# Optimization experiments

Measured on AMD Instinct MI355X. Metric: run time of the kernel, lower is better.

The kernel has to match this reference:

```python
import jax, jax.numpy as jnp
import numpy as np

THRESHOLD = 0.05
TOP_N = 300
NMS_THR = 0.6
POST_TOP_N = 100
MIN_SIZE = 0
N_CLASS = 81
C = N_CLASS - 1
STRIDES = (8, 16, 32, 64, 128)
IMG_H, IMG_W = 800, 1024
B = 16


def _level_hw(s):
    return (-(-IMG_H // s), -(-IMG_W // s))


def setup_inputs() -> dict:
    key = jax.random.key(0)
    inp = {}
    for li, s in enumerate(STRIDES):
        H, W = _level_hw(s)
        key, k1, k2, k3 = jax.random.split(key, 4)
        xs = (jnp.arange(W, dtype=jnp.float32) + 0.5) * s
        ys = (jnp.arange(H, dtype=jnp.float32) + 0.5) * s
        gx, gy = jnp.meshgrid(xs, ys)  # [H, W], row-major h*W+w flatten order
        inp[f"location{li}"] = jnp.stack([gx.reshape(-1), gy.reshape(-1)], -1)
        inp[f"cls{li}"] = jax.random.normal(k1, (B, C, H, W), jnp.float32)
        inp[f"box{li}"] = jax.random.uniform(k2, (B, 4, H, W), jnp.float32) * (4.0 * s)
        inp[f"ctr{li}"] = jax.random.normal(k3, (B, 1, H, W), jnp.float32)
    inp["img_h"] = IMG_H
    inp["img_w"] = IMG_W
    return inp


def _process_level(loc, cls, box, ctr, img_h, img_w):
    b, c, h, w = cls.shape
    cls = jax.nn.sigmoid(cls.transpose(0, 2, 3, 1).reshape(b, h * w, c))
    box = box.transpose(0, 2, 3, 1).reshape(b, h * w, 4)
    ctr = jax.nn.sigmoid(ctr.reshape(b, h * w))
    score = cls * ctr[:, :, None]                 # [B, HW, C]
    masked = jnp.where(cls > THRESHOLD, score, -1.0).reshape(b, -1)
    k = min(TOP_N, masked.shape[1])
    vals, idx = jax.lax.top_k(masked, k)
    if k < TOP_N:
        vals = jnp.pad(vals, ((0, 0), (0, TOP_N - k)), constant_values=-1.0)
        idx = jnp.pad(idx, ((0, 0), (0, TOP_N - k)))
    valid = vals > 0.0                            # candidates only; pads invalid
    pos = idx // c
    label = idx % c + 1
    ssel = jnp.take_along_axis(score.reshape(b, -1), idx, axis=1)  # differentiable gather
    bsel = jnp.take_along_axis(box, pos[..., None], axis=1)        # [B, TOP_N, 4]
    lsel = loc[pos]                                                # [B, TOP_N, 2]
    # decode + clip (BoxList.clip clamps to [0, size-1])
    x1 = jnp.clip(lsel[..., 0] - bsel[..., 0], 0.0, img_w - 1.0)
    y1 = jnp.clip(lsel[..., 1] - bsel[..., 1], 0.0, img_h - 1.0)
    x2 = jnp.clip(lsel[..., 0] + bsel[..., 2], 0.0, img_w - 1.0)
    y2 = jnp.clip(lsel[..., 1] + bsel[..., 3], 0.0, img_h - 1.0)
    det = jnp.stack([x1, y1, x2, y2], -1)
    # remove_small_box: xywh with remove=1
    valid = valid & ((x2 - x1 + 1.0) >= MIN_SIZE) & ((y2 - y1 + 1.0) >= MIN_SIZE)
    scores = jnp.sqrt(jnp.maximum(ssel, 1e-12))
    return det, scores, label, valid


def _pairwise_iou(b):
    area = (b[:, 2] - b[:, 0]) * (b[:, 3] - b[:, 1])
    lt = jnp.maximum(b[:, None, :2], b[None, :, :2])
    rb = jnp.minimum(b[:, None, 2:], b[None, :, 2:])
    wh = jnp.clip(rb - lt, 0.0)
    inter = wh[..., 0] * wh[..., 1]
    union = area[:, None] + area[None, :] - inter
    return inter / jnp.maximum(union, 1e-9)


def _nms_image(boxes, scores, labels, valid, offset):
    # per-class NMS via class-offset trick: boxes of different labels never overlap
    K = boxes.shape[0]
    s = jnp.where(valid, scores, -jnp.inf)
    order = jnp.argsort(-s)
    b = boxes[order]
    v = valid[order]
    lab = labels[order]
    so = s[order]
    iou = _pairwise_iou(b + (lab.astype(b.dtype) * offset)[:, None])
    ar = jnp.arange(K)

    def body(i, keep):
        sup = (iou[i] > NMS_THR) & keep[i] & (ar > i)
        return keep & ~sup

    keep = jax.lax.fori_loop(0, K, body, v)
    s2 = jnp.where(keep, so, -jnp.inf)
    _, idx2 = jax.lax.top_k(s2, POST_TOP_N)   # post_top_n selection
    fvalid = jnp.take(keep, idx2)
    fb = jnp.where(fvalid[:, None], b[idx2], 0.0)
    fs = jnp.where(fvalid, so[idx2], 0.0)
    fl = jnp.where(fvalid, lab[idx2], 0)
    return fb, fs, fl, fvalid


def _forward(locs, clss, boxs, ctrs, img_h, img_w):
    dets, scs, labs, vals = [], [], [], []
    for loc, cl, bx, ct in zip(locs, clss, boxs, ctrs):
        d, s, l, v = _process_level(loc, cl, bx, ct, float(img_h), float(img_w))
        dets.append(d); scs.append(s); labs.append(l); vals.append(v)
    det = jnp.concatenate(dets, 1)   # [B, 5*TOP_N, 4]
    sc = jnp.concatenate(scs, 1)
    lab = jnp.concatenate(labs, 1)
    val = jnp.concatenate(vals, 1)
    offset = float(max(img_h, img_w) + 1)
    fb, fs, fl, fv = jax.vmap(lambda b_, s_, l_, v_: _nms_image(b_, s_, l_, v_, offset))(det, sc, lab, val)
    out5 = jnp.concatenate([fb, fs[..., None]], -1)  # [B, POST_TOP_N, 5]
    return out5, fl, fv


def reference(location0, location1, location2, location3, location4,
              cls0, cls1, cls2, cls3, cls4,
              box0, box1, box2, box3, box4,
              ctr0, ctr1, ctr2, ctr3, ctr4,
              img_h, img_w):
    locs = [location0, location1, location2, location3, location4]
    clss = [cls0, cls1, cls2, cls3, cls4]
    boxs = [box0, box1, box2, box3, box4]
    ctrs = [ctr0, ctr1, ctr2, ctr3, ctr4]
    return _forward(locs, clss, boxs, ctrs, img_h, img_w)
```

## Files before the change

### kernel.cpp

```cpp
#include <hip/hip_runtime.h>
#include <math.h>

#define THREADS 256

constexpr int NLEV  = 5;
constexpr int NB    = 16;
constexpr int NC    = 80;
constexpr int TOPN  = 300;
constexpr int KC    = NLEV * TOPN;
constexpr int KROWS = 1536;
constexpr int WORDS = 24;
constexpr int NTRI  = WORDS * (WORDS + 1) / 2;
constexpr int POSTN = 100;
constexpr int CAP   = 4096;
constexpr int NBINS = 2048;
constexpr int NPAIR = NLEV * NB;

constexpr int HW0 = 12800, HW1 = 3200, HW2 = 800, HW3 = 208, HW4 = 56;
constexpr int CH0 = 63, CH1 = 16, CH2 = 4, CH3 = 2, CH4 = 1;
constexpr int CHUNKS = CH0 + CH1 + CH2 + CH3 + CH4;

constexpr int GPL0 = 4000, GPL1 = 1000, GPL2 = 250, GPL3 = 65, GPL4 = 18;
constexpr int GMXB0 = 0;
constexpr int GMXB1 = GMXB0 + NB * GPL0;
constexpr int GMXB2 = GMXB1 + NB * GPL1;
constexpr int GMXB3 = GMXB2 + NB * GPL2;
constexpr int GMXB4 = GMXB3 + NB * GPL3;
constexpr int GMXN  = GMXB4 + NB * GPL4;

constexpr int BPP = 16;

constexpr int HF_BIG = 1024, HF_SMALL = 1;

constexpr size_t align256(size_t x) { return (x + 255) & ~(size_t)255; }
constexpr size_t OFF_HIST = 0;
constexpr size_t OFF_CNT  = OFF_HIST + (size_t)NPAIR * NBINS * 4;
constexpr size_t OFF_CAND = align256(OFF_CNT + (size_t)NPAIR * 4);
constexpr size_t OFF_CBOX = align256(OFF_CAND + (size_t)NPAIR * CAP * 8);
constexpr size_t OFF_CSC  = align256(OFF_CBOX + (size_t)NB * KC * 4 * 4);
constexpr size_t OFF_CLB  = align256(OFF_CSC  + (size_t)NB * KC * 4);
constexpr size_t OFF_SSC  = align256(OFF_CLB  + (size_t)NB * KC * 4);
constexpr size_t OFF_SLB  = align256(OFF_SSC  + (size_t)NB * KC * 4);
constexpr size_t OFF_SBOX = align256(OFF_SLB  + (size_t)NB * KC * 4);
constexpr size_t OFF_OBOX = align256(OFF_SBOX + (size_t)NB * KC * 4 * 4);
constexpr size_t OFF_M    = align256(OFF_OBOX + (size_t)NB * KC * 4 * 4);
constexpr size_t OFF_GMX  = align256(OFF_M + (size_t)NB * KROWS * WORDS * 8);

struct Cand { float s; int i; };

__device__ __forceinline__ float sigm(float x) { return 1.0f / (1.0f + expf(-x)); }

__device__ __forceinline__ float sigf(float x) {
#if __has_builtin(__builtin_amdgcn_exp2f) && __has_builtin(__builtin_amdgcn_rcpf)
    float e = __builtin_amdgcn_exp2f(__fmul_rn(x, -1.44269504088896340736f));
    return __builtin_amdgcn_rcpf(__fadd_rn(1.0f, e));
#else
    return 1.0f / (1.0f + __expf(-x));
#endif
}

// ... 8 lines not shown
    unsigned hi = (unsigned)__builtin_amdgcn_readlane((int)(unsigned)(v >> 32), l);
    return ((unsigned long long)hi << 32) | lo;
}

__device__ void bitonicShared(float* ss, int* si, int N) {
    for (int k = 2; k <= N; k <<= 1) {
        for (int j = k >> 1; j > 0; j >>= 1) {
            __syncthreads();
            for (int i = threadIdx.x; i < N; i += blockDim.x) {
                int ixj = i ^ j;
                if (ixj > i) {
                    float s1 = ss[i], s2 = ss[ixj];
                    int a1 = si[i], a2 = si[ixj];
                    bool bef = (s1 > s2) || (s1 == s2 && a1 < a2);
                    bool up = ((i & k) == 0);
                    if (up ? !bef : bef) { ss[i] = s2; ss[ixj] = s1; si[i] = a2; si[ixj] = a1; }
                }
            }
        }
    }
    __syncthreads();
}

__global__ __launch_bounds__(THREADS) void k_zero(unsigned* __restrict__ zp, int zn) {
    int i = blockIdx.x * THREADS + threadIdx.x;
    if (i < zn) zp[i] = 0;
}

template<int HW, int GPL, int GMXB, int HF>
__device__ __forceinline__ void histChunkV(int chunkLocal, int b,
        const float* __restrict__ cls, const float* __restrict__ ctr,
        unsigned short* __restrict__ gmx, unsigned* __restrict__ h) {
    constexpr int NE = HW * NC;
    const float* cp = cls + (size_t)b * NE;
    const float* tb = ctr + (size_t)b * HW;
    unsigned short* gp = gmx + GMXB + (size_t)b * GPL;
    int w = threadIdx.x >> 6, lane = threadIdx.x & 63;
    int half = lane >> 5, hlane = lane & 31;
    for (int bi = w; bi < 32; bi += 4) {
        int ebase = (chunkLocal * 32 + bi) * 512;
        if (ebase >= NE) break;
        int e = ebase + lane * 8;
        int kmax = 0;
        if (e < NE) {
            int c = e / HW; int hwb = e - c * HW;
            float4 xa = *(const float4*)(cp + e);
            float4 xb = *(const float4*)(cp + e + 4);
            float4 ta = *(const float4*)(tb + hwb);
            float4 tc = *(const float4*)(tb + hwb + 4);
            float xs[8] = {xa.x, xa.y, xa.z, xa.w, xb.x, xb.y, xb.z, xb.w};
            float ts[8] = {ta.x, ta.y, ta.z, ta.w, tc.x, tc.y, tc.z, tc.w};
            #pragma unroll
            for (int q = 0; q < 8; ++q) {
                float scls = sigf(xs[q]);
                float s = __fmul_rn(scls, sigf(ts[q]));
                unsigned key = scoreKey(s);
                if (key >= (unsigned)HF) atomicAdd(&h[key], 1u);
                kmax = max(kmax, (int)key);
            }
        }
        #pragma unroll
        for (int sh = 1; sh < 32; sh <<= 1) kmax = max(kmax, __shfl_xor(kmax, sh, 64));
        int g = (ebase >> 8) + half;
        if (hlane == 0 && g * 256 < NE) gp[g] = (unsigned short)kmax;
    }
}

__global__ __launch_bounds__(THREADS) void k_hist(
        const float* c0, const float* c1, const float* c2, const float* c3, const float* c4,
        const float* t0, const float* t1, const float* t2, const float* t3, const float* t4,
        unsigned short* __restrict__ gmx, unsigned* ghist) {
    __shared__ unsigned h[NBINS];
    for (int k = threadIdx.x; k < NBINS; k += THREADS) h[k] = 0;
    __syncthreads();
    int cx = blockIdx.x, b = blockIdx.y;
    int li;
    if (cx < CH0)                 { histChunkV<HW0,GPL0,GMXB0,HF_BIG>(cx, b, c0, t0, gmx, h); li = 0; }
    else if (cx < CH0+CH1)        { histChunkV<HW1,GPL1,GMXB1,HF_BIG>(cx-CH0, b, c1, t1, gmx, h); li = 1; }
    else if (cx < CH0+CH1+CH2)    { histChunkV<HW2,GPL2,GMXB2,HF_BIG>(cx-CH0-CH1, b, c2, t2, gmx, h); li = 2; }
    else if (cx < CH0+CH1+CH2+CH3){ histChunkV<HW3,GPL3,GMXB3,HF_SMALL>(cx-CH0-CH1-CH2, b, c3, t3, gmx, h); li = 3; }
    else                          { histChunkV<HW4,GPL4,GMXB4,HF_SMALL>(cx-CH0-CH1-CH2-CH3, b, c4, t4, gmx, h); li = 4; }
    __syncthreads();
    unsigned* gp = ghist + (size_t)(li * NB + b) * NBINS;
    for (int k = threadIdx.x; k < NBINS; k += THREADS) {
        unsigned v = h[k];
        if (v) atomicAdd(&gp[k], v);
    }
}

constexpr int LBUF = 1024;
constexpr int GB = 8;

template<int HW>
__device__ __forceinline__ void procList(int b, int pid, unsigned Tv, unsigned n,
        const unsigned short* __restrict__ glist,
        const float* __restrict__ cls, const float* __restrict__ ctr,
        Cand* __restrict__ cd, unsigned* __restrict__ cnt,
        Cand* __restrict__ lbuf, unsigned* __restrict__ lcnt) {
    constexpr int NE = HW * NC;
    const float* cp = cls + (size_t)b * NE;
    const float* tb = ctr + (size_t)b * HW;
    for (unsigned base = 0; base < n; base += GB) {
        float xv[GB], rv[GB];
        int ev[GB];
        bool okv[GB];
        #pragma unroll
        for (int q = 0; q < GB; ++q) {
            unsigned gi = base + q;
            int g = glist[(gi < n) ? gi : (n - 1)];
            int e = g * 256 + (int)threadIdx.x;
            bool ok = (gi < n) && (e < NE);
            e = ok ? e : 0;
// ... 4 lines not shown
            okv[q] = ok;
        }
        __builtin_amdgcn_sched_barrier(0);
        #pragma unroll
        for (int q = 0; q < GB; ++q) {
            float scls = sigm(xv[q]);
            float s = __fmul_rn(scls, sigm(rv[q]));
            unsigned key = scoreKey(s);
            bool take = okv[q] && (Tv ? (key >= Tv) : (scls > 0.05f));
            if (take) {
                int e = ev[q];
                int c = e / HW; int hw = e - c * HW;
                unsigned slot = atomicAdd(lcnt, 1u);
                if (slot < (unsigned)LBUF) { lbuf[slot].s = s; lbuf[slot].i = hw * NC + c; }
                else {
                    unsigned gs = atomicAdd(&cnt[pid], 1u);
                    if (gs < (unsigned)CAP) { cd[gs].s = s; cd[gs].i = hw * NC + c; }
                }
            }
        }
    }
}

__global__ __launch_bounds__(THREADS) void k_collect(
        const float* c0, const float* c1, const float* c2, const float* c3, const float* c4,
        const float* t0, const float* t1, const float* t2, const float* t3, const float* t4,
        const unsigned* __restrict__ ghist, const unsigned short* __restrict__ gmx,
        Cand* cand, unsigned* cnt) {
    __shared__ unsigned sfx[THREADS];
    __shared__ int tstar;
    __shared__ unsigned shTv;
    __shared__ Cand lbuf[LBUF];
    __shared__ unsigned lcnt, gbase, gcnt;
    __shared__ unsigned short glist[THREADS];
    int tid = (int)threadIdx.x;
    int pid = blockIdx.y;
    int li = pid >> 4, b = pid & 15;
    if (tid == 0) { lcnt = 0; gcnt = 0; tstar = -1; }

    const unsigned* h = ghist + (size_t)pid * NBINS;
    unsigned s = 0;
    #pragma unroll
    for (int k = 0; k < 8; ++k) s += h[tid * 8 + k];
    sfx[tid] = s;
    for (int d = 1; d < THREADS; d <<= 1) {
        __syncthreads();
        unsigned v = (tid + d < THREADS) ? sfx[tid + d] : 0u;
        __syncthreads();
        sfx[tid] += v;
    }
    __syncthreads();
    if (sfx[tid] >= (unsigned)TOPN && (tid == THREADS - 1 || sfx[tid + 1] < (unsigned)TOPN))
        tstar = tid;
    __syncthreads();
    if (tid == 0) {
        unsigned TA = 0;
        int t = tstar;
        if (t >= 0) {
            unsigned acc = (t < THREADS - 1) ? sfx[t + 1] : 0u;
            int lo = t * 8, bin = lo + 7;
            for (; bin >= lo; --bin) { acc += h[bin]; if (acc >= (unsigned)TOPN) break; }
            TA = (unsigned)max(bin, lo);
        }
        shTv = (TA >= 1) ? (TA - 1) : 0u;
    }
    __syncthreads();
    unsigned Tv = shTv;

    int GPL, GMXB;
    switch (li) {
        case 0: GPL = GPL0; GMXB = GMXB0; break;
        case 1: GPL = GPL1; GMXB = GMXB1; break;
        case 2: GPL = GPL2; GMXB = GMXB2; break;
        case 3: GPL = GPL3; GMXB = GMXB3; break;
        default: GPL = GPL4; GMXB = GMXB4; break;
    }
    const unsigned short* gp = gmx + GMXB + (size_t)b * GPL;
    int per = (GPL + BPP - 1) / BPP;
    int lo = (int)blockIdx.x * per;
    int hi = min(GPL, lo + per);
    {
        int g = lo + tid;
        bool ok = (g < hi);
        if (ok && Tv) ok = ((unsigned)gp[g] + 1u >= Tv);
        unsigned long long m = __ballot(ok);
        int nW = __popcll(m);
        if (nW) {
            unsigned wb = 0;
            if ((tid & 63) == 0) wb = atomicAdd(&gcnt, (unsigned)nW);
            wb = (unsigned)__builtin_amdgcn_readfirstlane((int)wb);
            if (ok) glist[wb + (unsigned)__popcll(m & ((1ull << (tid & 63)) - 1ull))] = (unsigned short)g;
        }
    }
    __syncthreads();
    unsigned n = gcnt;
    Cand* cd = cand + (size_t)pid * CAP;
    if (n) {
        switch (li) {
            case 0: procList<HW0>(b, pid, Tv, n, glist, c0, t0, cd, cnt, lbuf, &lcnt); break;
            case 1: procList<HW1>(b, pid, Tv, n, glist, c1, t1, cd, cnt, lbuf, &lcnt); break;
            case 2: procList<HW2>(b, pid, Tv, n, glist, c2, t2, cd, cnt, lbuf, &lcnt); break;
            case 3: procList<HW3>(b, pid, Tv, n, glist, c3, t3, cd, cnt, lbuf, &lcnt); break;
            default: procList<HW4>(b, pid, Tv, n, glist, c4, t4, cd, cnt, lbuf, &lcnt); break;
        }
    }
    __syncthreads();
    unsigned nl = lcnt; if (nl > (unsigned)LBUF) nl = LBUF;
    if (tid == 0) gbase = nl ? atomicAdd(&cnt[pid], nl) : 0u;
    __syncthreads();
    for (unsigned i = tid; i < nl; i += THREADS) {
        unsigned sl = gbase + i;
        if (sl < (unsigned)CAP) cd[sl] = lbuf[i];
    }
}

__global__ __launch_bounds__(THREADS) void k_select(
        const Cand* __restrict__ candAll, const unsigned* __restrict__ cntAll,
        const float* l0, const float* l1, const float* l2, const float* l3, const float* l4,
        const float* b0, const float* b1, const float* b2, const float* b3, const float* b4,
        float* __restrict__ cbox, float* __restrict__ csc, int* __restrict__ clb) {
    __shared__ float ss[CAP];
    __shared__ int si[CAP];
    int pid = blockIdx.x;
    int li = pid / NB, b = pid - li * NB;
    int n = (int)min(cntAll[pid], (unsigned)CAP);
    const Cand* cd = candAll + (size_t)pid * CAP;
    int N = 2; while (N < n) N <<= 1;
    for (int k = threadIdx.x; k < N; k += THREADS) {
        if (k < n) { ss[k] = cd[k].s; si[k] = cd[k].i; }
        else       { ss[k] = -INFINITY; si[k] = 0x40000000 + k; }
    }
    __syncthreads();
    bitonicShared(ss, si, N);

    const float* locp; const float* boxp; int HW;
    switch (li) {
        case 0: locp = l0; boxp = b0; HW = HW0; break;
        case 1: locp = l1; boxp = b1; HW = HW1; break;
        case 2: locp = l2; boxp = b2; HW = HW2; break;
        case 3: locp = l3; boxp = b3; HW = HW3; break;
        default: locp = l4; boxp = b4; HW = HW4; break;
    }
    for (int j = threadIdx.x; j < TOPN; j += THREADS) {
        int cidx = b * KC + li * TOPN + j;
        bool ok = (j < n);
        float s = ok ? ss[j] : -INFINITY;
        ok = ok && (s > 0.0f);
        if (ok) {
            int idx = si[j];
            int hw = idx / NC, c = idx - hw * NC;
            float lx = locp[hw * 2 + 0], ly = locp[hw * 2 + 1];
            const float* bp = boxp + (size_t)b * 4 * HW + hw;
            float bl = bp[0], bt = bp[HW], br = bp[2 * HW], bb = bp[3 * HW];
            float x1 = fminf(fmaxf(__fsub_rn(lx, bl), 0.0f), 1023.0f);
            float y1 = fminf(fmaxf(__fsub_rn(ly, bt), 0.0f),  799.0f);
            float x2 = fminf(fmaxf(__fadd_rn(lx, br), 0.0f), 1023.0f);
            float y2 = fminf(fmaxf(__fadd_rn(ly, bb), 0.0f),  799.0f);
            cbox[cidx * 4 + 0] = x1; cbox[cidx * 4 + 1] = y1;
            cbox[cidx * 4 + 2] = x2; cbox[cidx * 4 + 3] = y2;
            csc[cidx] = sqrtf(fmaxf(s, 1e-12f));
            clb[cidx] = c + 1;
        } else {
            cbox[cidx * 4 + 0] = 0.0f; cbox[cidx * 4 + 1] = 0.0f;
            cbox[cidx * 4 + 2] = 0.0f; cbox[cidx * 4 + 3] = 0.0f;
            csc[cidx] = -INFINITY;
            clb[cidx] = 0;
        }
    }
}

__global__ __launch_bounds__(THREADS) void k_merge(
        const float* __restrict__ csc, const int* __restrict__ clb, const float* __restrict__ cbox,
        float* __restrict__ ssc, int* __restrict__ slb, float* __restrict__ sbox,
        float* __restrict__ obox) {
    int li = blockIdx.x, b = blockIdx.y;
    __shared__ float ss[KC];
    for (int k = threadIdx.x; k < KC; k += THREADS) ss[k] = csc[b * KC + k];
    __syncthreads();
    for (int j = threadIdx.x; j < TOPN; j += THREADS) {
        int k = li * TOPN + j;
        float s = ss[k];
        int rank = j;
        #pragma unroll
        for (int l = 0; l < NLEV; ++l) {
            if (l == li) continue;
            const float* seg = ss + l * TOPN;
            int lo = 0, hi = TOPN;
            if (l < li) {
                while (lo < hi) { int m = (lo + hi) >> 1; if (seg[m] >= s) lo = m + 1; else hi = m; }
            } else {
                while (lo < hi) { int m = (lo + hi) >> 1; if (seg[m] >  s) lo = m + 1; else hi = m; }
            }
            rank += lo;
        }
        int src = b * KC + k, dst = b * KC + rank;
        int lab = clb[src];
        ssc[dst] = s; slb[dst] = lab;
        float off = __fmul_rn((float)lab, 1025.0f);
        float4 v = *(const float4*)&cbox[(size_t)src * 4];
        *(float4*)&sbox[(size_t)dst * 4] = v;
        float4 o;
        o.x = __fadd_rn(v.x, off); o.y = __fadd_rn(v.y, off);
        o.z = __fadd_rn(v.z, off); o.w = __fadd_rn(v.w, off);
        *(float4*)&obox[(size_t)dst * 4] = o;
    }
}

__global__ __launch_bounds__(64) void k_iou(const float* __restrict__ obox,
                                            unsigned long long* __restrict__ MT) {
    int t = blockIdx.x, b = blockIdx.y;
    int tile = 0, rem = t;
    while (rem >= WORDS - tile) { rem -= WORDS - tile; ++tile; }
    int w = tile + rem;
    int lane = threadIdx.x;
    __shared__ float4 sj[64];
    __shared__ float aj[64];
    const float4* op = (const float4*)obox + (size_t)b * KC;
    int j0 = w * 64;
    int jl = j0 + lane;
    float4 vj = op[(jl < KC) ? jl : (KC - 1)];
    sj[lane] = vj;
    aj[lane] = __fmul_rn(__fsub_rn(vj.z, vj.x), __fsub_rn(vj.w, vj.y));
    int i = tile * 64 + lane;
    float4 bi = op[(i < KC) ? i : (KC - 1)];
    float ai = __fmul_rn(__fsub_rn(bi.z, bi.x), __fsub_rn(bi.w, bi.y));
    __syncthreads();
    unsigned long long bits = 0;
    int jmax = min(64, KC - j0);
    for (int jj = 0; jj < jmax; ++jj) {
        float4 bj = sj[jj];
        float xx1 = fmaxf(bi.x, bj.x), yy1 = fmaxf(bi.y, bj.y);
        float xx2 = fminf(bi.z, bj.z), yy2 = fminf(bi.w, bj.w);
        float ww = fmaxf(__fsub_rn(xx2, xx1), 0.0f);
        float hh = fmaxf(__fsub_rn(yy2, yy1), 0.0f);
        float inter = __fmul_rn(ww, hh);
        float uni = __fsub_rn(__fadd_rn(ai, aj[jj]), inter);
        float iou = __fdiv_rn(inter, fmaxf(uni, 1e-9f));
        bool kp = ((j0 + jj) > i) && (iou > 0.6f);
        bits |= kp ? (1ull << jj) : 0ull;
    }
    if (i >= KC) bits = 0;
    MT[((size_t)b * WORDS + w) * KROWS + i] = bits;
}

__global__ __launch_bounds__(64) void k_nms(
        const unsigned long long* __restrict__ MT, const float* __restrict__ ssc,
        const int* __restrict__ slb, const float* __restrict__ sbox, float* __restrict__ out) {
    int b = blockIdx.x, lane = threadIdx.x;
    for (int k = lane; k < POSTN * 5; k += 64) out[(size_t)b * POSTN * 5 + k] = 0.0f;
    for (int k = lane; k < POSTN; k += 64) {
        out[(size_t)NB * POSTN * 5 + b * POSTN + k] = 0.0f;
        out[(size_t)NB * POSTN * 5 + NB * POSTN + b * POSTN + k] = 0.0f;
    }
    const float* sp = ssc + b * KC;
    unsigned long long validV = 0;
    for (int c = 0; c < WORDS; ++c) {
        int i = c * 64 + lane;
        bool f = (i < KC) && (sp[i] > 0.0f);
        unsigned long long m = __ballot(f);
        validV = (lane == c) ? m : validV;
    }
    unsigned long long mybit = 1ull << lane;
    unsigned long long keptV = 0;
    const unsigned long long* Mb = MT + (size_t)b * WORDS * KROWS;

    unsigned long long pv[WORDS];
    pv[0] = Mb[lane];

    int keptTotal = 0;
    for (int t = 0; t < WORDS; ++t) {
        int tn = (t + 1 < WORDS) ? (t + 1) : t;
        const unsigned long long* cp = Mb + (size_t)tn * KROWS + lane;
        unsigned long long nv[WORDS];
        #pragma unroll
        for (int c = 0; c < WORDS; ++c) {
            int cc = (c <= tn) ? c : 0;
            nv[c] = cp[(size_t)cc * 64];
        }
        __builtin_amdgcn_sched_barrier(0);

        unsigned long long D = pv[t];
        unsigned long long acc = 0;
        #pragma unroll
        for (int c = 0; c < WORDS; ++c) {
            if (c < t) {
                unsigned long long kc = readlane64(keptV, c);
                if (kc & mybit) acc |= pv[c];
            }
        }
        #pragma unroll
        for (int s = 1; s < 64; s <<= 1) acc |= __shfl_xor(acc, s, 64);

        unsigned long long validT = readlane64(validV, t);
        unsigned long long rem = acc;
        unsigned long long sup = __ballot(D != 0ull) & validT;
        unsigned long long todoS = sup;
        while (todoS) {
            int r = __builtin_ctzll(todoS);
            todoS &= todoS - 1;
            if (!((rem >> r) & 1ull)) {
                unsigned long long Dr = readlane64(D, r);
                rem |= Dr;
                todoS &= ~Dr;
            }
        }
        unsigned long long kept = validT & ~rem;
        keptV = (lane == t) ? kept : keptV;

        keptTotal += (int)__popcll(kept);
        if (keptTotal >= POSTN) break;

        #pragma unroll
        for (int c = 0; c < WORDS; ++c) pv[c] = nv[c];
    }

    int base = 0;
    for (int c = 0; c < WORDS && base < POSTN; ++c) {
        unsigned long long kw = readlane64(keptV, c);
        bool f = (kw & mybit) != 0ull;
        int rank = base + __popcll(kw & (mybit - 1ull));
        if (f && rank < POSTN) {
            int i = c * 64 + lane;
            int src = b * KC + i;
            float* o5 = out + ((size_t)b * POSTN + rank) * 5;
            o5[0] = sbox[src * 4 + 0]; o5[1] = sbox[src * 4 + 1];
            o5[2] = sbox[src * 4 + 2]; o5[3] = sbox[src * 4 + 3];
            o5[4] = ssc[src];
            out[(size_t)NB * POSTN * 5 + b * POSTN + rank] = (float)slb[src];
            out[(size_t)NB * POSTN * 5 + NB * POSTN + b * POSTN + rank] = 1.0f;
        }
        base += __popcll(kw);
    }
}

extern "C" void kernel_launch(void* const* d_in, const int* in_sizes, int n_in,
                              void* d_out, int out_size, void* d_ws, size_t ws_size,
                              hipStream_t stream) {
    const float *loc[5], *cls[5], *box[5], *ctr[5];
    for (int l = 0; l < 5; ++l) {
        loc[l] = (const float*)d_in[l * 4 + 0];
        cls[l] = (const float*)d_in[l * 4 + 1];
        box[l] = (const float*)d_in[l * 4 + 2];
        ctr[l] = (const float*)d_in[l * 4 + 3];
    }
    char* ws = (char*)d_ws;
    unsigned* hist = (unsigned*)(ws + OFF_HIST);
    unsigned* cnt  = (unsigned*)(ws + OFF_CNT);
    Cand* cand     = (Cand*)(ws + OFF_CAND);
    float* cbox    = (float*)(ws + OFF_CBOX);
    float* csc     = (float*)(ws + OFF_CSC);
    int*   clb     = (int*)(ws + OFF_CLB);
    float* ssc     = (float*)(ws + OFF_SSC);
    int*   slb     = (int*)(ws + OFF_SLB);
    float* sbox    = (float*)(ws + OFF_SBOX);
    float* obox    = (float*)(ws + OFF_OBOX);
    unsigned long long* MT = (unsigned long long*)(ws + OFF_M);
    unsigned short* gmx = (unsigned short*)(ws + OFF_GMX);
    float* out = (float*)d_out;

    int zn = (int)(OFF_CAND / 4);
    k_zero<<<(zn + THREADS - 1) / THREADS, THREADS, 0, stream>>>((unsigned*)ws, zn);
    k_hist<<<dim3(CHUNKS, NB), THREADS, 0, stream>>>(
        cls[0], cls[1], cls[2], cls[3], cls[4],
        ctr[0], ctr[1], ctr[2], ctr[3], ctr[4], gmx, hist);
    k_collect<<<dim3(BPP, NPAIR), THREADS, 0, stream>>>(
        cls[0], cls[1], cls[2], cls[3], cls[4],
        ctr[0], ctr[1], ctr[2], ctr[3], ctr[4], hist, gmx, cand, cnt);
    k_select<<<NPAIR, THREADS, 0, stream>>>(
        cand, cnt,
        loc[0], loc[1], loc[2], loc[3], loc[4],
        box[0], box[1], box[2], box[3], box[4],
        cbox, csc, clb);
    k_merge<<<dim3(NLEV, NB), THREADS, 0, stream>>>(csc, clb, cbox, ssc, slb, sbox, obox);
    k_iou<<<dim3(NTRI, NB), 64, 0, stream>>>(obox, MT);
    k_nms<<<NB, 64, 0, stream>>>(MT, ssc, slb, sbox, out);
}
```

Measured before the change: 240.2 us.

## Fuse pipeline stages into a persistent megakernel with hierarchical grid barriers

New measurement: 783.1 us. 226% more time.

```diff
diff --git a/kernel.cpp b/kernel.cpp
--- a/kernel.cpp
+++ b/kernel.cpp
@@ -30,12 +30,18 @@
 
 constexpr int BPP = 16;
 
+constexpr int NBLK   = 1024;
+constexpr int LEAVES = 64;
+constexpr int BPL    = NBLK / LEAVES;
+
 constexpr int HF_BIG = 1024, HF_SMALL = 1;
 
 constexpr size_t align256(size_t x) { return (x + 255) & ~(size_t)255; }
 constexpr size_t OFF_HIST = 0;
 constexpr size_t OFF_CNT  = OFF_HIST + (size_t)NPAIR * NBINS * 4;
-constexpr size_t OFF_CAND = align256(OFF_CNT + (size_t)NPAIR * 4);
+constexpr size_t OFF_BAR  = OFF_CNT + (size_t)NPAIR * 4;
+constexpr size_t BARWORDS = 1056;
+constexpr size_t OFF_CAND = align256(OFF_BAR + BARWORDS * 4);
 constexpr size_t OFF_CBOX = align256(OFF_CAND + (size_t)NPAIR * CAP * 8);
 constexpr size_t OFF_CSC  = align256(OFF_CBOX + (size_t)NB * KC * 4 * 4);
 constexpr size_t OFF_CLB  = align256(OFF_CSC  + (size_t)NB * KC * 4);
@@ -90,9 +96,25 @@
     __syncthreads();
 }
 
-__global__ __launch_bounds__(THREADS) void k_zero(unsigned* __restrict__ zp, int zn) {
-    int i = blockIdx.x * THREADS + threadIdx.x;
-    if (i < zn) zp[i] = 0;
+__device__ __forceinline__ void gridBar(unsigned* bar, int phase) {
+    __syncthreads();
+    if (threadIdx.x == 0) {
+        __threadfence();
+        int leaf = (int)(blockIdx.x & (LEAVES - 1));
+        unsigned v = __hip_atomic_fetch_add(&bar[leaf * 16], 1u,
+                        __ATOMIC_ACQ_REL, __HIP_MEMORY_SCOPE_AGENT);
+        if (v == (unsigned)(BPL * (phase + 1) - 1)) {
+            unsigned r = __hip_atomic_fetch_add(&bar[1024], 1u,
+                            __ATOMIC_ACQ_REL, __HIP_MEMORY_SCOPE_AGENT);
+            if (r == (unsigned)(LEAVES * (phase + 1) - 1))
+                __hip_atomic_store(&bar[1040], (unsigned)(phase + 1),
+                                   __ATOMIC_RELEASE, __HIP_MEMORY_SCOPE_AGENT);
+        }
+        while (__hip_atomic_load(&bar[1040], __ATOMIC_ACQUIRE, __HIP_MEMORY_SCOPE_AGENT)
+               < (unsigned)(phase + 1))
+            __builtin_amdgcn_s_sleep(8);
+    }
+    __syncthreads();
 }
 
 template<int HW, int GPL, int GMXB, int HF>
@@ -134,28 +156,6 @@
     }
 }
 
-__global__ __launch_bounds__(THREADS) void k_hist(
-        const float* c0, const float* c1, const float* c2, const float* c3, const float* c4,
-        const float* t0, const float* t1, const float* t2, const float* t3, const float* t4,
-        unsigned short* __restrict__ gmx, unsigned* ghist) {
-    __shared__ unsigned h[NBINS];
-    for (int k = threadIdx.x; k < NBINS; k += THREADS) h[k] = 0;
-    __syncthreads();
-    int cx = blockIdx.x, b = blockIdx.y;
-    int li;
-    if (cx < CH0)                 { histChunkV<HW0,GPL0,GMXB0,HF_BIG>(cx, b, c0, t0, gmx, h); li = 0; }
-    else if (cx < CH0+CH1)        { histChunkV<HW1,GPL1,GMXB1,HF_BIG>(cx-CH0, b, c1, t1, gmx, h); li = 1; }
-    else if (cx < CH0+CH1+CH2)    { histChunkV<HW2,GPL2,GMXB2,HF_BIG>(cx-CH0-CH1, b, c2, t2, gmx, h); li = 2; }
-    else if (cx < CH0+CH1+CH2+CH3){ histChunkV<HW3,GPL3,GMXB3,HF_SMALL>(cx-CH0-CH1-CH2, b, c3, t3, gmx, h); li = 3; }
-    else                          { histChunkV<HW4,GPL4,GMXB4,HF_SMALL>(cx-CH0-CH1-CH2-CH3, b, c4, t4, gmx, h); li = 4; }
-    __syncthreads();
-    unsigned* gp = ghist + (size_t)(li * NB + b) * NBINS;
-    for (int k = threadIdx.x; k < NBINS; k += THREADS) {
-        unsigned v = h[k];
-        if (v) atomicAdd(&gp[k], v);
-    }
-}
-
 constexpr int LBUF = 1024;
 constexpr int GB = 8;
 
@@ -206,314 +206,368 @@
     }
 }
 
-__global__ __launch_bounds__(THREADS) void k_collect(
+__global__ __launch_bounds__(THREADS) void k_zero(unsigned* __restrict__ zp, int zn) {
+    int i = blockIdx.x * THREADS + threadIdx.x;
+    if (i < zn) zp[i] = 0;
+}
+
+__global__ __launch_bounds__(THREADS, 4) void k_mega(
+        const float* l0, const float* l1, const float* l2, const float* l3, const float* l4,
         const float* c0, const float* c1, const float* c2, const float* c3, const float* c4,
+        const float* b0, const float* b1, const float* b2, const float* b3, const float* b4,
         const float* t0, const float* t1, const float* t2, const float* t3, const float* t4,
-        const unsigned* __restrict__ ghist, const unsigned short* __restrict__ gmx,
-        Cand* cand, unsigned* cnt) {
-    __shared__ unsigned sfx[THREADS];
+        char* __restrict__ ws, float* __restrict__ out) {
+    __shared__ __align__(16) char smem[32768];
+    __shared__ unsigned shTv, lcnt, gbase, gcnt;
     __shared__ int tstar;
-    __shared__ unsigned shTv;
-    __shared__ Cand lbuf[LBUF];
-    __shared__ unsigned lcnt, gbase, gcnt;
-    __shared__ unsigned short glist[THREADS];
-    int tid = (int)threadIdx.x;
-    int pid = blockIdx.y;
-    int li = pid >> 4, b = pid & 15;
-    if (tid == 0) { lcnt = 0; gcnt = 0; tstar = -1; }
-
-    const unsigned* h = ghist + (size_t)pid * NBINS;
-    unsigned s = 0;
-    #pragma unroll
-    for (int k = 0; k < 8; ++k) s += h[tid * 8 + k];
-    sfx[tid] = s;
-    for (int d = 1; d < THREADS; d <<= 1) {
-        __syncthreads();
-        unsigned v = (tid + d < THREADS) ? sfx[tid + d] : 0u;
-        __syncthreads();
-        sfx[tid] += v;
-    }
-    __syncthreads();
-    if (sfx[tid] >= (unsigned)TOPN && (tid == THREADS - 1 || sfx[tid + 1] < (unsigned)TOPN))
-        tstar = tid;
-    __syncthreads();
-    if (tid == 0) {
-        unsigned TA = 0;
-        int t = tstar;
-        if (t >= 0) {
-            unsigned acc = (t < THREADS - 1) ? sfx[t + 1] : 0u;
-            int lo = t * 8, bin = lo + 7;
-            for (; bin >= lo; --bin) { acc += h[bin]; if (acc >= (unsigned)TOPN) break; }
-            TA = (unsigned)max(bin, lo);
-        }
-        shTv = (TA >= 1) ? (TA - 1) : 0u;
-    }
-    __syncthreads();
-    unsigned Tv = shTv;
-
-    int GPL, GMXB;
-    switch (li) {
-        case 0: GPL = GPL0; GMXB = GMXB0; break;
-        case 1: GPL = GPL1; GMXB = GMXB1; break;
-        case 2: GPL = GPL2; GMXB = GMXB2; break;
-        case 3: GPL = GPL3; GMXB = GMXB3; break;
-        default: GPL = GPL4; GMXB = GMXB4; break;
-    }
-    const unsigned short* gp = gmx + GMXB + (size_t)b * GPL;
-    int per = (GPL + BPP - 1) / BPP;
-    int lo = (int)blockIdx.x * per;
-    int hi = min(GPL, lo + per);
+
+    unsigned* ghist = (unsigned*)(ws + OFF_HIST);
+    unsigned* cnt   = (unsigned*)(ws + OFF_CNT);
+    unsigned* bar   = (unsigned*)(ws + OFF_BAR);
+    Cand* cand      = (Cand*)(ws + OFF_CAND);
+    float* cbox     = (float*)(ws + OFF_CBOX);
+    float* csc      = (float*)(ws + OFF_CSC);
+    int*   clb      = (int*)(ws + OFF_CLB);
+    float* ssc      = (float*)(ws + OFF_SSC);
+    int*   slb      = (int*)(ws + OFF_SLB);
+    float* sbox     = (float*)(ws + OFF_SBOX);
+    float* obox     = (float*)(ws + OFF_OBOX);
+    unsigned long long* MT = (unsigned long long*)(ws + OFF_M);
+    unsigned short* gmx = (unsigned short*)(ws + OFF_GMX);
+
+    const int tid = (int)threadIdx.x;
+    const int bid = (int)blockIdx.x;
+
     {
-        int g = lo + tid;
-        bool ok = (g < hi);
-        if (ok && Tv) ok = ((unsigned)gp[g] + 1u >= Tv);
-        unsigned long long m = __ballot(ok);
-        int nW = __popcll(m);
-        if (nW) {
-            unsigned wb = 0;
-            if ((tid & 63) == 0) wb = atomicAdd(&gcnt, (unsigned)nW);
-            wb = (unsigned)__builtin_amdgcn_readfirstlane((int)wb);
-            if (ok) glist[wb + (unsigned)__popcll(m & ((1ull << (tid & 63)) - 1ull))] = (unsigned short)g;
-        }
-    }
-    __syncthreads();
-    unsigned n = gcnt;
-    Cand* cd = cand + (size_t)pid * CAP;
-    if (n) {
-        switch (li) {
-            case 0: procList<HW0>(b, pid, Tv, n, glist, c0, t0, cd, cnt, lbuf, &lcnt); break;
-            case 1: procList<HW1>(b, pid, Tv, n, glist, c1, t1, cd, cnt, lbuf, &lcnt); break;
-            case 2: procList<HW2>(b, pid, Tv, n, glist, c2, t2, cd, cnt, lbuf, &lcnt); break;
-            case 3: procList<HW3>(b, pid, Tv, n, glist, c3, t3, cd, cnt, lbuf, &lcnt); break;
-            default: procList<HW4>(b, pid, Tv, n, glist, c4, t4, cd, cnt, lbuf, &lcnt); break;
-        }
-    }
-    __syncthreads();
-    unsigned nl = lcnt; if (nl > (unsigned)LBUF) nl = LBUF;
-    if (tid == 0) gbase = nl ? atomicAdd(&cnt[pid], nl) : 0u;
-    __syncthreads();
-    for (unsigned i = tid; i < nl; i += THREADS) {
-        unsigned sl = gbase + i;
-        if (sl < (unsigned)CAP) cd[sl] = lbuf[i];
-    }
-}
-
-__global__ __launch_bounds__(THREADS) void k_select(
-        const Cand* __restrict__ candAll, const unsigned* __restrict__ cntAll,
-        const float* l0, const float* l1, const float* l2, const float* l3, const float* l4,
-        const float* b0, const float* b1, const float* b2, const float* b3, const float* b4,
-        float* __restrict__ cbox, float* __restrict__ csc, int* __restrict__ clb) {
-    __shared__ float ss[CAP];
-    __shared__ int si[CAP];
-    int pid = blockIdx.x;
-    int li = pid / NB, b = pid - li * NB;
-    int n = (int)min(cntAll[pid], (unsigned)CAP);
-    const Cand* cd = candAll + (size_t)pid * CAP;
-    int N = 2; while (N < n) N <<= 1;
-    for (int k = threadIdx.x; k < N; k += THREADS) {
-        if (k < n) { ss[k] = cd[k].s; si[k] = cd[k].i; }
-        else       { ss[k] = -INFINITY; si[k] = 0x40000000 + k; }
-    }
-    __syncthreads();
-    bitonicShared(ss, si, N);
-
-    const float* locp; const float* boxp; int HW;
-    switch (li) {
-        case 0: locp = l0; boxp = b0; HW = HW0; break;
-        case 1: locp = l1; boxp = b1; HW = HW1; break;
-        case 2: locp = l2; boxp = b2; HW = HW2; break;
-        case 3: locp = l3; boxp = b3; HW = HW3; break;
-        default: locp = l4; boxp = b4; HW = HW4; break;
-    }
-    for (int j = threadIdx.x; j < TOPN; j += THREADS) {
-        int cidx = b * KC + li * TOPN + j;
-        bool ok = (j < n);
-        float s = ok ? ss[j] : -INFINITY;
-        ok = ok && (s > 0.0f);
-        if (ok) {
-            int idx = si[j];
-            int hw = idx / NC, c = idx - hw * NC;
-            float lx = locp[hw * 2 + 0], ly = locp[hw * 2 + 1];
-            const float* bp = boxp + (size_t)b * 4 * HW + hw;
-            float bl = bp[0], bt = bp[HW], br = bp[2 * HW], bb = bp[3 * HW];
-            float x1 = fminf(fmaxf(__fsub_rn(lx, bl), 0.0f), 1023.0f);
-            float y1 = fminf(fmaxf(__fsub_rn(ly, bt), 0.0f),  799.0f);
-            float x2 = fminf(fmaxf(__fadd_rn(lx, br), 0.0f), 1023.0f);
-            float y2 = fminf(fmaxf(__fadd_rn(ly, bb), 0.0f),  799.0f);
-            cbox[cidx * 4 + 0] = x1; cbox[cidx * 4 + 1] = y1;
-            cbox[cidx * 4 + 2] = x2; cbox[cidx * 4 + 3] = y2;
-            csc[cidx] = sqrtf(fmaxf(s, 1e-12f));
-            clb[cidx] = c + 1;
-        } else {
-            cbox[cidx * 4 + 0] = 0.0f; cbox[cidx * 4 + 1] = 0.0f;
-            cbox[cidx * 4 + 2] = 0.0f; cbox[cidx * 4 + 3] = 0.0f;
-            csc[cidx] = -INFINITY;
-            clb[cidx] = 0;
-        }
-    }
-}
-
-__global__ __launch_bounds__(THREADS) void k_merge(
-        const float* __restrict__ csc, const int* __restrict__ clb, const float* __restrict__ cbox,
-        float* __restrict__ ssc, int* __restrict__ slb, float* __restrict__ sbox,
-        float* __restrict__ obox) {
-    int li = blockIdx.x, b = blockIdx.y;
-    __shared__ float ss[KC];
-    for (int k = threadIdx.x; k < KC; k += THREADS) ss[k] = csc[b * KC + k];
-    __syncthreads();
-    for (int j = threadIdx.x; j < TOPN; j += THREADS) {
-        int k = li * TOPN + j;
-        float s = ss[k];
-        int rank = j;
-        #pragma unroll
-        for (int l = 0; l < NLEV; ++l) {
-            if (l == li) continue;
-            const float* seg = ss + l * TOPN;
-            int lo = 0, hi = TOPN;
-            if (l < li) {
-                while (lo < hi) { int m = (lo + hi) >> 1; if (seg[m] >= s) lo = m + 1; else hi = m; }
-            } else {
-                while (lo < hi) { int m = (lo + hi) >> 1; if (seg[m] >  s) lo = m + 1; else hi = m; }
-            }
-            rank += lo;
-        }
-        int src = b * KC + k, dst = b * KC + rank;
-        int lab = clb[src];
-        ssc[dst] = s; slb[dst] = lab;
-        float off = __fmul_rn((float)lab, 1025.0f);
-        float4 v = *(const float4*)&cbox[(size_t)src * 4];
-        *(float4*)&sbox[(size_t)dst * 4] = v;
-        float4 o;
-        o.x = __fadd_rn(v.x, off); o.y = __fadd_rn(v.y, off);
-        o.z = __fadd_rn(v.z, off); o.w = __fadd_rn(v.w, off);
-        *(float4*)&obox[(size_t)dst * 4] = o;
-    }
-}
-
-__global__ __launch_bounds__(64) void k_iou(const float* __restrict__ obox,
-                                            unsigned long long* __restrict__ MT) {
-    int t = blockIdx.x, b = blockIdx.y;
-    int tile = 0, rem = t;
-    while (rem >= WORDS - tile) { rem -= WORDS - tile; ++tile; }
-    int w = tile + rem;
-    int lane = threadIdx.x;
-    __shared__ float4 sj[64];
-    __shared__ float aj[64];
-    const float4* op = (const float4*)obox + (size_t)b * KC;
-    int j0 = w * 64;
-    int jl = j0 + lane;
-    float4 vj = op[(jl < KC) ? jl : (KC - 1)];
-    sj[lane] = vj;
-    aj[lane] = __fmul_rn(__fsub_rn(vj.z, vj.x), __fsub_rn(vj.w, vj.y));
-    int i = tile * 64 + lane;
-    float4 bi = op[(i < KC) ? i : (KC - 1)];
-    float ai = __fmul_rn(__fsub_rn(bi.z, bi.x), __fsub_rn(bi.w, bi.y));
-    __syncthreads();
-    unsigned long long bits = 0;
-    int jmax = min(64, KC - j0);
-    for (int jj = 0; jj < jmax; ++jj) {
-        float4 bj = sj[jj];
-        float xx1 = fmaxf(bi.x, bj.x), yy1 = fmaxf(bi.y, bj.y);
-        float xx2 = fminf(bi.z, bj.z), yy2 = fminf(bi.w, bj.w);
-        float ww = fmaxf(__fsub_rn(xx2, xx1), 0.0f);
-        float hh = fmaxf(__fsub_rn(yy2, yy1), 0.0f);
-        float inter = __fmul_rn(ww, hh);
-        float uni = __fsub_rn(__fadd_rn(ai, aj[jj]), inter);
-        float iou = __fdiv_rn(inter, fmaxf(uni, 1e-9f));
-        bool kp = ((j0 + jj) > i) && (iou > 0.6f);
-        bits |= kp ? (1ull << jj) : 0ull;
-    }
-    if (i >= KC) bits = 0;
-    MT[((size_t)b * WORDS + w) * KROWS + i] = bits;
-}
-
-__global__ __launch_bounds__(64) void k_nms(
-        const unsigned long long* __restrict__ MT, const float* __restrict__ ssc,
-        const int* __restrict__ slb, const float* __restrict__ sbox, float* __restrict__ out) {
-    int b = blockIdx.x, lane = threadIdx.x;
-    for (int k = lane; k < POSTN * 5; k += 64) out[(size_t)b * POSTN * 5 + k] = 0.0f;
-    for (int k = lane; k < POSTN; k += 64) {
-        out[(size_t)NB * POSTN * 5 + b * POSTN + k] = 0.0f;
-        out[(size_t)NB * POSTN * 5 + NB * POSTN + b * POSTN + k] = 0.0f;
-    }
-    const float* sp = ssc + b * KC;
-    unsigned long long validV = 0;
-    for (int c = 0; c < WORDS; ++c) {
-        int i = c * 64 + lane;
-        bool f = (i < KC) && (sp[i] > 0.0f);
-        unsigned long long m = __ballot(f);
-        validV = (lane == c) ? m : validV;
-    }
-    unsigned long long mybit = 1ull << lane;
-    unsigned long long keptV = 0;
-    const unsigned long long* Mb = MT + (size_t)b * WORDS * KROWS;
-
-    unsigned long long pv[WORDS];
-    pv[0] = Mb[lane];
-
-    int keptTotal = 0;
-    for (int t = 0; t < WORDS; ++t) {
-        int tn = (t + 1 < WORDS) ? (t + 1) : t;
-        const unsigned long long* cp = Mb + (size_t)tn * KROWS + lane;
-        unsigned long long nv[WORDS];
-        #pragma unroll
+        unsigned* h = (unsigned*)smem;
+        for (int item = bid; item < CHUNKS * NB; item += NBLK) {
+            __syncthreads();
+            for (int k = tid; k < NBINS; k += THREADS) h[k] = 0;
+            __syncthreads();
+            int cx = item % CHUNKS, b = item / CHUNKS;
+            int li;
+            if (cx < CH0)                 { histChunkV<HW0,GPL0,GMXB0,HF_BIG>(cx, b, c0, t0, gmx, h); li = 0; }
+            else if (cx < CH0+CH1)        { histChunkV<HW1,GPL1,GMXB1,HF_BIG>(cx-CH0, b, c1, t1, gmx, h); li = 1; }
+            else if (cx < CH0+CH1+CH2)    { histChunkV<HW2,GPL2,GMXB2,HF_BIG>(cx-CH0-CH1, b, c2, t2, gmx, h); li = 2; }
+            else if (cx < CH0+CH1+CH2+CH3){ histChunkV<HW3,GPL3,GMXB3,HF_SMALL>(cx-CH0-CH1-CH2, b, c3, t3, gmx, h); li = 3; }
+            else                          { histChunkV<HW4,GPL4,GMXB4,HF_SMALL>(cx-CH0-CH1-CH2-CH3, b, c4, t4, gmx, h); li = 4; }
+            __syncthreads();
+            unsigned* gp = ghist + (size_t)(li * NB + b) * NBINS;
+            for (int k = tid; k < NBINS; k += THREADS) {
+                unsigned v = h[k];
+                if (v) atomicAdd(&gp[k], v);
+            }
+        }
+    }
+    gridBar(bar, 0);
+
+    {
+        unsigned* sfx = (unsigned*)smem;
+        Cand* lbuf = (Cand*)(smem + 1024);
+        unsigned short* glist = (unsigned short*)(smem + 9216);
+        for (int item = bid; item < BPP * NPAIR; item += NBLK) {
+            __syncthreads();
+            if (tid == 0) { lcnt = 0; gcnt = 0; tstar = -1; }
+            int pid = item % NPAIR;
+            int bx  = item / NPAIR;
+            int li = pid >> 4, b = pid & 15;
+            const unsigned* h = ghist + (size_t)pid * NBINS;
+            unsigned s = 0;
+            #pragma unroll
+            for (int k = 0; k < 8; ++k) s += h[tid * 8 + k];
+            sfx[tid] = s;
+            for (int d = 1; d < THREADS; d <<= 1) {
+                __syncthreads();
+                unsigned v = (tid + d < THREADS) ? sfx[tid + d] : 0u;
+                __syncthreads();
+                sfx[tid] += v;
+            }
+            __syncthreads();
+            if (sfx[tid] >= (unsigned)TOPN && (tid == THREADS - 1 || sfx[tid + 1] < (unsigned)TOPN))
+                tstar = tid;
+            __syncthreads();
+            if (tid == 0) {
+                unsigned TA = 0;
+                int t = tstar;
+                if (t >= 0) {
+                    unsigned acc = (t < THREADS - 1) ? sfx[t + 1] : 0u;
+                    int lo = t * 8, bin = lo + 7;
+                    for (; bin >= lo; --bin) { acc += h[bin]; if (acc >= (unsigned)TOPN) break; }
+                    TA = (unsigned)max(bin, lo);
+                }
+                shTv = (TA >= 1) ? (TA - 1) : 0u;
+            }
+            __syncthreads();
+            unsigned Tv = shTv;
+            int GPL, GMXB;
+            switch (li) {
+                case 0: GPL = GPL0; GMXB = GMXB0; break;
+                case 1: GPL = GPL1; GMXB = GMXB1; break;
+                case 2: GPL = GPL2; GMXB = GMXB2; break;
+                case 3: GPL = GPL3; GMXB = GMXB3; break;
+                default: GPL = GPL4; GMXB = GMXB4; break;
+            }
+            const unsigned short* gp = gmx + GMXB + (size_t)b * GPL;
+            int per = (GPL + BPP - 1) / BPP;
+            int lo = bx * per;
+            int hi = min(GPL, lo + per);
+            {
+                int g = lo + tid;
+                bool ok = (g < hi);
+                if (ok && Tv) ok = ((unsigned)gp[g] + 1u >= Tv);
+                unsigned long long m = __ballot(ok);
+                int nW = __popcll(m);
+                if (nW) {
+                    unsigned wb = 0;
+                    if ((tid & 63) == 0) wb = atomicAdd(&gcnt, (unsigned)nW);
+                    wb = (unsigned)__builtin_amdgcn_readfirstlane((int)wb);
+                    if (ok) glist[wb + (unsigned)__popcll(m & ((1ull << (tid & 63)) - 1ull))] = (unsigned short)g;
+                }
+            }
+            __syncthreads();
+            unsigned n = gcnt;
+            Cand* cd = cand + (size_t)pid * CAP;
+            if (n) {
+                switch (li) {
+                    case 0: procList<HW0>(b, pid, Tv, n, glist, c0, t0, cd, cnt, lbuf, &lcnt); break;
+                    case 1: procList<HW1>(b, pid, Tv, n, glist, c1, t1, cd, cnt, lbuf, &lcnt); break;
+                    case 2: procList<HW2>(b, pid, Tv, n, glist, c2, t2, cd, cnt, lbuf, &lcnt); break;
+                    case 3: procList<HW3>(b, pid, Tv, n, glist, c3, t3, cd, cnt, lbuf, &lcnt); break;
+                    default: procList<HW4>(b, pid, Tv, n, glist, c4, t4, cd, cnt, lbuf, &lcnt); break;
+                }
+            }
+            __syncthreads();
+            unsigned nl = lcnt; if (nl > (unsigned)LBUF) nl = LBUF;
+            if (tid == 0) gbase = nl ? atomicAdd(&cnt[pid], nl) : 0u;
+            __syncthreads();
+            for (unsigned i = tid; i < nl; i += THREADS) {
+                unsigned sl = gbase + i;
+                if (sl < (unsigned)CAP) cd[sl] = lbuf[i];
+            }
+        }
+    }
+    gridBar(bar, 1);
+
+    {
+        float* ss = (float*)smem;
+        int* si = (int*)(smem + 16384);
+        for (int pid = bid; pid < NPAIR; pid += NBLK) {
+            int li = pid / NB, b = pid - li * NB;
+            int n = (int)min(cnt[pid], (unsigned)CAP);
+            const Cand* cd = cand + (size_t)pid * CAP;
+            int N = 2; while (N < n) N <<= 1;
+            for (int k = tid; k < N; k += THREADS) {
+                if (k < n) { ss[k] = cd[k].s; si[k] = cd[k].i; }
+                else       { ss[k] = -INFINITY; si[k] = 0x40000000 + k; }
+            }
+            __syncthreads();
+            bitonicShared(ss, si, N);
+            const float* locp; const float* boxp; int HW;
+            switch (li) {
+                case 0: locp = l0; boxp = b0; HW = HW0; break;
+                case 1: locp = l1; boxp = b1; HW = HW1; break;
+                case 2: locp = l2; boxp = b2; HW = HW2; break;
+                case 3: locp = l3; boxp = b3; HW = HW3; break;
+                default: locp = l4; boxp = b4; HW = HW4; break;
+            }
+            for (int j = tid; j < TOPN; j += THREADS) {
+                int cidx = b * KC + li * TOPN + j;
+                bool ok = (j < n);
+                float s = ok ? ss[j] : -INFINITY;
+                ok = ok && (s > 0.0f);
+                if (ok) {
+                    int idx = si[j];
+                    int hw = idx / NC, c = idx - hw * NC;
+                    float lx = locp[hw * 2 + 0], ly = locp[hw * 2 + 1];
+                    const float* bp = boxp + (size_t)b * 4 * HW + hw;
+                    float bl = bp[0], bt = bp[HW], br = bp[2 * HW], bb = bp[3 * HW];
+                    float x1 = fminf(fmaxf(__fsub_rn(lx, bl), 0.0f), 1023.0f);
+                    float y1 = fminf(fmaxf(__fsub_rn(ly, bt), 0.0f),  799.0f);
+                    float x2 = fminf(fmaxf(__fadd_rn(lx, br), 0.0f), 1023.0f);
+                    float y2 = fminf(fmaxf(__fadd_rn(ly, bb), 0.0f),  799.0f);
+                    cbox[cidx * 4 + 0] = x1; cbox[cidx * 4 + 1] = y1;
+                    cbox[cidx * 4 + 2] = x2; cbox[cidx * 4 + 3] = y2;
+                    csc[cidx] = sqrtf(fmaxf(s, 1e-12f));
+                    clb[cidx] = c + 1;
+                } else {
+                    cbox[cidx * 4 + 0] = 0.0f; cbox[cidx * 4 + 1] = 0.0f;
+                    cbox[cidx * 4 + 2] = 0.0f; cbox[cidx * 4 + 3] = 0.0f;
+                    csc[cidx] = -INFINITY;
+                    clb[cidx] = 0;
+                }
+            }
+            __syncthreads();
+        }
+    }
+    gridBar(bar, 2);
+
+    {
+        float* ms = (float*)smem;
+        for (int item = bid; item < NLEV * NB; item += NBLK) {
+            int li = item % NLEV, b = item / NLEV;
+            for (int k = tid; k < KC; k += THREADS) ms[k] = csc[b * KC + k];
+            __syncthreads();
+            for (int j = tid; j < TOPN; j += THREADS) {
+                int k = li * TOPN + j;
+                float s = ms[k];
+                int rank = j;
+                #pragma unroll
+                for (int l = 0; l < NLEV; ++l) {
+                    if (l == li) continue;
+                    const float* seg = ms + l * TOPN;
+                    int lo = 0, hi = TOPN;
+                    if (l < li) {
+                        while (lo < hi) { int m = (lo + hi) >> 1; if (seg[m] >= s) lo = m + 1; else hi = m; }
+                    } else {
+                        while (lo < hi) { int m = (lo + hi) >> 1; if (seg[m] >  s) lo = m + 1; else hi = m; }
+                    }
+                    rank += lo;
+                }
+                int src = b * KC + k, dst = b * KC + rank;
+                int lab = clb[src];
+                ssc[dst] = s; slb[dst] = lab;
+                float off = __fmul_rn((float)lab, 1025.0f);
+                float4 v = *(const float4*)&cbox[(size_t)src * 4];
+                *(float4*)&sbox[(size_t)dst * 4] = v;
+                float4 o;
+                o.x = __fadd_rn(v.x, off); o.y = __fadd_rn(v.y, off);
+                o.z = __fadd_rn(v.z, off); o.w = __fadd_rn(v.w, off);
+                *(float4*)&obox[(size_t)dst * 4] = o;
+            }
+            __syncthreads();
+        }
+    }
+    gridBar(bar, 3);
+
+    {
+        float4* sj = (float4*)smem;
+        float*  aj = (float*)(smem + 4096);
+        int wid = tid >> 6, lane = tid & 63;
+        float4* sjW = sj + wid * 64;
+        float*  ajW = aj + wid * 64;
+        for (int base = bid * 4; base < NTRI * NB; base += NBLK * 4) {
+            int wit = base + wid;
+            bool act = (wit < NTRI * NB);
+            int t = act ? (wit % NTRI) : 0;
+            int b = act ? (wit / NTRI) : 0;
+            int tile = 0, rem = t;
+            while (rem >= WORDS - tile) { rem -= WORDS - tile; ++tile; }
+            int w = tile + rem;
+            const float4* op = (const float4*)obox + (size_t)b * KC;
+            int j0 = w * 64;
+            int jl = j0 + lane;
+            float4 vj = op[(jl < KC) ? jl : (KC - 1)];
+            sjW[lane] = vj;
+            ajW[lane] = __fmul_rn(__fsub_rn(vj.z, vj.x), __fsub_rn(vj.w, vj.y));
+            int i = tile * 64 + lane;
+            float4 bi = op[(i < KC) ? i : (KC - 1)];
+            float ai = __fmul_rn(__fsub_rn(bi.z, bi.x), __fsub_rn(bi.w, bi.y));
+            unsigned long long bits = 0;
+            int jmax = min(64, KC - j0);
+            for (int jj = 0; jj < jmax; ++jj) {
+                float4 bj = sjW[jj];
+                float xx1 = fmaxf(bi.x, bj.x), yy1 = fmaxf(bi.y, bj.y);
+                float xx2 = fminf(bi.z, bj.z), yy2 = fminf(bi.w, bj.w);
+                float ww = fmaxf(__fsub_rn(xx2, xx1), 0.0f);
+                float hh = fmaxf(__fsub_rn(yy2, yy1), 0.0f);
+                float inter = __fmul_rn(ww, hh);
+                float uni = __fsub_rn(__fadd_rn(ai, ajW[jj]), inter);
+                float iou = __fdiv_rn(inter, fmaxf(uni, 1e-9f));
+                bool kp = ((j0 + jj) > i) && (iou > 0.6f);
+                bits |= kp ? (1ull << jj) : 0ull;
+            }
+            if (i >= KC) bits = 0;
+            if (act) MT[((size_t)b * WORDS + w) * KROWS + i] = bits;
+        }
+    }
+    gridBar(bar, 4);
+
+    if (bid < NB && tid < 64) {
+        int b = bid, lane = tid;
+        for (int k = lane; k < POSTN * 5; k += 64) out[(size_t)b * POSTN * 5 + k] = 0.0f;
+        for (int k = lane; k < POSTN; k += 64) {
+            out[(size_t)NB * POSTN * 5 + b * POSTN + k] = 0.0f;
+            out[(size_t)NB * POSTN * 5 + NB * POSTN + b * POSTN + k] = 0.0f;
+        }
+        const float* sp = ssc + b * KC;
+        unsigned long long validV = 0;
         for (int c = 0; c < WORDS; ++c) {
-            int cc = (c <= tn) ? c : 0;
-            nv[c] = cp[(size_t)cc * 64];
-        }
-        __builtin_amdgcn_sched_barrier(0);
-
-        unsigned long long D = pv[t];
-        unsigned long long acc = 0;
-        #pragma unroll
-        for (int c = 0; c < WORDS; ++c) {
-            if (c < t) {
-                unsigned long long kc = readlane64(keptV, c);
-                if (kc & mybit) acc |= pv[c];
-            }
-        }
-        #pragma unroll
-        for (int s = 1; s < 64; s <<= 1) acc |= __shfl_xor(acc, s, 64);
-
-        unsigned long long validT = readlane64(validV, t);
-        unsigned long long rem = acc;
-        unsigned long long sup = __ballot(D != 0ull) & validT;
-        unsigned long long todoS = sup;
-        while (todoS) {
-            int r = __builtin_ctzll(todoS);
-            todoS &= todoS - 1;
-            if (!((rem >> r) & 1ull)) {
-                unsigned long long Dr = readlane64(D, r);
-                rem |= Dr;
-                todoS &= ~Dr;
-            }
-        }
-        unsigned long long kept = validT & ~rem;
-        keptV = (lane == t) ? kept : keptV;
-
-        keptTotal += (int)__popcll(kept);
-        if (keptTotal >= POSTN) break;
-
-        #pragma unroll
-        for (int c = 0; c < WORDS; ++c) pv[c] = nv[c];
-    }
-
-    int base = 0;
-    for (int c = 0; c < WORDS && base < POSTN; ++c) {
-        unsigned long long kw = readlane64(keptV, c);
-        bool f = (kw & mybit) != 0ull;
-        int rank = base + __popcll(kw & (mybit - 1ull));
-        if (f && rank < POSTN) {
             int i = c * 64 + lane;
-            int src = b * KC + i;
-            float* o5 = out + ((size_t)b * POSTN + rank) * 5;
-            o5[0] = sbox[src * 4 + 0]; o5[1] = sbox[src * 4 + 1];
-            o5[2] = sbox[src * 4 + 2]; o5[3] = sbox[src * 4 + 3];
-            o5[4] = ssc[src];
-            out[(size_t)NB * POSTN * 5 + b * POSTN + rank] = (float)slb[src];
-            out[(size_t)NB * POSTN * 5 + NB * POSTN + b * POSTN + rank] = 1.0f;
-        }
-        base += __popcll(kw);
+            bool f = (i < KC) && (sp[i] > 0.0f);
+            unsigned long long m = __ballot(f);
+            validV = (lane == c) ? m : validV;
+        }
+        unsigned long long mybit = 1ull << lane;
+        unsigned long long keptV = 0;
+        const unsigned long long* Mb = MT + (size_t)b * WORDS * KROWS;
+
+        unsigned long long pv[WORDS];
+        pv[0] = Mb[lane];
+
+        int keptTotal = 0;
+        for (int t = 0; t < WORDS; ++t) {
+            int tn = (t + 1 < WORDS) ? (t + 1) : t;
+            const unsigned long long* cp = Mb + (size_t)tn * KROWS + lane;
+            unsigned long long nv[WORDS];
+            #pragma unroll
+            for (int c = 0; c < WORDS; ++c) {
+                int cc = (c <= tn) ? c : 0;
+                nv[c] = cp[(size_t)cc * 64];
+            }
+            __builtin_amdgcn_sched_barrier(0);
+
+            unsigned long long D = pv[t];
+            unsigned long long acc = 0;
+            #pragma unroll
+            for (int c = 0; c < WORDS; ++c) {
+                if (c < t) {
+                    unsigned long long kc = readlane64(keptV, c);
+                    if (kc & mybit) acc |= pv[c];
+                }
+            }
+            #pragma unroll
+            for (int s = 1; s < 64; s <<= 1) acc |= __shfl_xor(acc, s, 64);
+
+            unsigned long long validT = readlane64(validV, t);
+            unsigned long long rem = acc;
+            unsigned long long sup = __ballot(D != 0ull) & validT;
+            unsigned long long todoS = sup;
+            while (todoS) {
+                int r = __builtin_ctzll(todoS);
+                todoS &= todoS - 1;
+                if (!((rem >> r) & 1ull)) {
+                    unsigned long long Dr = readlane64(D, r);
+                    rem |= Dr;
+                    todoS &= ~Dr;
+                }
+            }
+            unsigned long long kept = validT & ~rem;
+            keptV = (lane == t) ? kept : keptV;
+
+            keptTotal += (int)__popcll(kept);
+            if (keptTotal >= POSTN) break;
+
+            #pragma unroll
+            for (int c = 0; c < WORDS; ++c) pv[c] = nv[c];
+        }
+
+        int base = 0;
+        for (int c = 0; c < WORDS && base < POSTN; ++c) {
+            unsigned long long kw = readlane64(keptV, c);
+            bool f = (kw & mybit) != 0ull;
+            int rank = base + __popcll(kw & (mybit - 1ull));
+            if (f && rank < POSTN) {
+                int i = c * 64 + lane;
+                int src = b * KC + i;
+                float* o5 = out + ((size_t)b * POSTN + rank) * 5;
+                o5[0] = sbox[src * 4 + 0]; o5[1] = sbox[src * 4 + 1];
+                o5[2] = sbox[src * 4 + 2]; o5[3] = sbox[src * 4 + 3];
+                o5[4] = ssc[src];
+                out[(size_t)NB * POSTN * 5 + b * POSTN + rank] = (float)slb[src];
+                out[(size_t)NB * POSTN * 5 + NB * POSTN + b * POSTN + rank] = 1.0f;
+            }
+            base += __popcll(kw);
+        }
     }
 }
 
@@ -528,34 +582,14 @@
         ctr[l] = (const float*)d_in[l * 4 + 3];
     }
     char* ws = (char*)d_ws;
-    unsigned* hist = (unsigned*)(ws + OFF_HIST);
-    unsigned* cnt  = (unsigned*)(ws + OFF_CNT);
-    Cand* cand     = (Cand*)(ws + OFF_CAND);
-    float* cbox    = (float*)(ws + OFF_CBOX);
-    float* csc     = (float*)(ws + OFF_CSC);
-    int*   clb     = (int*)(ws + OFF_CLB);
-    float* ssc     = (float*)(ws + OFF_SSC);
-    int*   slb     = (int*)(ws + OFF_SLB);
-    float* sbox    = (float*)(ws + OFF_SBOX);
-    float* obox    = (float*)(ws + OFF_OBOX);
-    unsigned long long* MT = (unsigned long long*)(ws + OFF_M);
-    unsigned short* gmx = (unsigned short*)(ws + OFF_GMX);
     float* out = (float*)d_out;
 
     int zn = (int)(OFF_CAND / 4);
     k_zero<<<(zn + THREADS - 1) / THREADS, THREADS, 0, stream>>>((unsigned*)ws, zn);
-    k_hist<<<dim3(CHUNKS, NB), THREADS, 0, stream>>>(
+    k_mega<<<NBLK, THREADS, 0, stream>>>(
+        loc[0], loc[1], loc[2], loc[3], loc[4],
         cls[0], cls[1], cls[2], cls[3], cls[4],
-        ctr[0], ctr[1], ctr[2], ctr[3], ctr[4], gmx, hist);
-    k_collect<<<dim3(BPP, NPAIR), THREADS, 0, stream>>>(
-        cls[0], cls[1], cls[2], cls[3], cls[4],
-        ctr[0], ctr[1], ctr[2], ctr[3], ctr[4], hist, gmx, cand, cnt);
-    k_select<<<NPAIR, THREADS, 0, stream>>>(
-        cand, cnt,
-        loc[0], loc[1], loc[2], loc[3], loc[4],
         box[0], box[1], box[2], box[3], box[4],
-        cbox, csc, clb);
-    k_merge<<<dim3(NLEV, NB), THREADS, 0, stream>>>(csc, clb, cbox, ssc, slb, sbox, obox);
-    k_iou<<<dim3(NTRI, NB), 64, 0, stream>>>(obox, MT);
-    k_nms<<<NB, 64, 0, stream>>>(MT, ssc, slb, sbox, out);
-}
+        ctr[0], ctr[1], ctr[2], ctr[3], ctr[4],
+        ws, out);
+}
```
